# Optimization experiments

Hardware: AMD Instinct MI355X
Metric: run time of the kernel (lower is better)

Reference implementation:

```python
import jax, jax.numpy as jnp
import numpy as np

D_PAIR = 128
D_HIDDEN = 128
EPS = 1e-5


def layer_norm(x, w, b):
    mu = jnp.mean(x, axis=-1, keepdims=True)
    var = jnp.var(x, axis=-1, keepdims=True)
    return (x - mu) * jax.lax.rsqrt(var + EPS) * w + b


def setup_inputs() -> dict:
    key = jax.random.key(0)
    ks = jax.random.split(key, 8)
    B, N, D, H = 1, 512, D_PAIR, D_HIDDEN
    pair = jax.random.normal(ks[0], (B, N, N, D), dtype=jnp.float32)
    # torch Linear weight layout: [out_features, in_features]
    p_in_w = jax.random.normal(ks[1], (2 * H, D), dtype=jnp.float32) / np.sqrt(D)
    g_in_w = jax.random.normal(ks[2], (2 * H, D), dtype=jnp.float32) / np.sqrt(D)
    p_out_w = jax.random.normal(ks[3], (D, H), dtype=jnp.float32) / np.sqrt(H)
    g_out_w = jax.random.normal(ks[4], (D, D), dtype=jnp.float32) / np.sqrt(D)
    ln_in_w = jnp.ones((D,), jnp.float32)
    ln_in_b = jnp.zeros((D,), jnp.float32)
    ln_out_w = jnp.ones((H,), jnp.float32)
    ln_out_b = jnp.zeros((H,), jnp.float32)
    return {
        "pair": pair,
        "ln_in_w": ln_in_w, "ln_in_b": ln_in_b,
        "p_in_w": p_in_w, "g_in_w": g_in_w,
        "ln_out_w": ln_out_w, "ln_out_b": ln_out_b,
        "p_out_w": p_out_w, "g_out_w": g_out_w,
    }


def reference(pair, ln_in_w, ln_in_b, p_in_w, g_in_w, ln_out_w, ln_out_b, p_out_w, g_out_w):
    H = D_HIDDEN
    L = pair.shape[1]
    pair_norm = layer_norm(pair, ln_in_w, ln_in_b)           # [B,N,N,D]
    p = jnp.einsum('bijd,hd->bijh', pair_norm, p_in_w)       # [B,N,N,2H]
    g = jax.nn.sigmoid(jnp.einsum('bijd,hd->bijh', pair_norm, g_in_w))
    left = g[..., :H] * p[..., :H]
    right = g[..., H:] * p[..., H:]
    # outgoing direction
    out = jnp.einsum('bikd,bjkd->bijd', left, right / jnp.float32(L))
    out = layer_norm(out, ln_out_w, ln_out_b)
    out = jnp.einsum('bijh,dh->bijd', out, p_out_w)
    gate = jax.nn.sigmoid(jnp.einsum('bijd,ed->bije', pair_norm, g_out_w))
    return gate * out
```

## Files before the change

kernel.cpp:

```cpp
#include <hip/hip_runtime.h>

#define NSEQ 512
#define RTOT (NSEQ*NSEQ)
#define DM 128

typedef unsigned short ushort_t;
using short8 = __attribute__((ext_vector_type(8))) short;
using f32x4  = __attribute__((ext_vector_type(4))) float;

__device__ __forceinline__ unsigned short f2bf(float x){
  union { float f; unsigned int u; } v; v.f = x;
  unsigned int r = v.u + 0x7fffu + ((v.u >> 16) & 1u);
  return (unsigned short)(r >> 16);
}
__device__ __forceinline__ float bf2f(unsigned short u){
  union { unsigned int u; float f; } v; v.u = ((unsigned int)u) << 16;
  return v.f;
}
__device__ __forceinline__ unsigned int pack2(float a, float b){
  return (unsigned int)f2bf(a) | ((unsigned int)f2bf(b) << 16);
}
__device__ __forceinline__ float sigmoidf(float x){ return 1.0f/(1.0f + __expf(-x)); }

__global__ __launch_bounds__(256) void k_prep(const float* __restrict__ a,
                                              const float* __restrict__ b,
                                              ushort_t* __restrict__ da,
                                              ushort_t* __restrict__ db,
                                              int na4, int nb4){
  int idx = blockIdx.x*256 + threadIdx.x;
  const float* src; ushort_t* dst; int i;
  if (idx < na4){ src = a; dst = da; i = idx; }
  else { i = idx - na4; if (i >= nb4) return; src = b; dst = db; }
  float4 v = *(const float4*)(src + (size_t)i*4);
  uint2 pk; pk.x = pack2(v.x, v.y); pk.y = pack2(v.z, v.w);
  *(uint2*)(dst + (size_t)i*4) = pk;
}

__global__ __launch_bounds__(256) void k_prep2(const float* __restrict__ p_out_w,
                                               const float* __restrict__ g_out_w,
                                               const float* __restrict__ ln_out_w,
                                               const float* __restrict__ ln_out_b,
                                               ushort_t* __restrict__ wp,
                                               ushort_t* __restrict__ wg,
                                               float2* __restrict__ c12){
  int t = threadIdx.x;
  if (t < 128){
    float s1 = 0.f, s2 = 0.f;
    for (int d = 0; d < DM; d++){
      float v = p_out_w[(size_t)t*DM + d];
      unsigned short h = f2bf(v * ln_out_w[d]);
      wp[(size_t)t*DM + d] = h;
      s1 += bf2f(h);
      s2 += ln_out_b[d] * v;
    }
    c12[t] = make_float2(s1, s2);
  } else {
    int r = t - 128;
    for (int d = 0; d < DM; d += 4){
      float4 v = *(const float4*)&g_out_w[(size_t)r*DM + d];
      uint2 pk; pk.x = pack2(v.x, v.y); pk.y = pack2(v.z, v.w);
      *(uint2*)&wg[(size_t)r*DM + d] = pk;
    }
  }
}

__global__ __launch_bounds__(256) void k0_ln_in(const float* __restrict__ pair,
                                                const float* __restrict__ w,
                                                const float* __restrict__ b,
                                                ushort_t* __restrict__ lnx){
  int wv = threadIdx.x >> 6, lane = threadIdx.x & 63;
  size_t row = (size_t)blockIdx.x * 4 + wv;
  const float2* src = (const float2*)(pair + row * DM);
  float2 v = src[lane];
  float s = v.x + v.y, s2 = v.x*v.x + v.y*v.y;
  #pragma unroll
  for (int off = 32; off; off >>= 1){ s += __shfl_xor(s, off); s2 += __shfl_xor(s2, off); }
  float mu = s * (1.f/DM);
  float rstd = rsqrtf(s2*(1.f/DM) - mu*mu + 1e-5f);
  float o0 = (v.x - mu)*rstd*w[2*lane]   + b[2*lane];
  float o1 = (v.y - mu)*rstd*w[2*lane+1] + b[2*lane+1];
  ((unsigned int*)(lnx + row * DM))[lane] = pack2(o0, o1);
}

__global__ __launch_bounds__(256) void k1_inproj(const ushort_t* __restrict__ lnx,
                                                 const ushort_t* __restrict__ pw_bf,
                                                 const ushort_t* __restrict__ gw_bf,
                                                 ushort_t* __restrict__ left,
                                                 ushort_t* __restrict__ right){
  int tid = threadIdx.x;
  int wc = tid >> 6, lane = tid & 63, m = lane & 15, quad = lane >> 4;
  int job = blockIdx.x;
  int wrow0 = ((job >= 2) ? 128 : 0) + (job & 1) * 64;
  ushort_t* outp = (job >= 2) ? right : left;
  int d = (job & 1) * 64 + wc*16 + m;
  size_t row0 = (size_t)blockIdx.y * 256;

  const ushort_t* prow = pw_bf + (size_t)(wrow0 + wc*16 + m)*DM + quad*8;
  const ushort_t* grow = gw_bf + (size_t)(wrow0 + wc*16 + m)*DM + quad*8;
  short8 bp[4], bg[4];
  #pragma unroll
  for (int k = 0; k < 4; k++){
    bp[k] = *(const short8*)(prow + k*32);
    bg[k] = *(const short8*)(grow + k*32);
  }

  #pragma unroll
  for (int ch = 0; ch < 4; ch++){
    size_t r0 = row0 + ch*64;
    f32x4 accp[4], accg[4];
    #pragma unroll
    for (int i = 0; i < 4; i++){ accp[i] = (f32x4){0.f,0.f,0.f,0.f}; accg[i] = (f32x4){0.f,0.f,0.f,0.f}; }
    #pragma unroll
    for (int k = 0; k < 4; k++){
      #pragma unroll
      for (int rt = 0; rt < 4; rt++){
        short8 a = *(const short8*)&lnx[(r0 + rt*16 + m)*DM + k*32 + quad*8];
        accp[rt] = __builtin_amdgcn_mfma_f32_16x16x32_bf16(a, bp[k], accp[rt], 0, 0, 0);
        accg[rt] = __builtin_amdgcn_mfma_f32_16x16x32_bf16(a, bg[k], accg[rt], 0, 0, 0);
      }
    }
    #pragma unroll
    for (int rt = 0; rt < 4; rt++){
      uint2 pk;
      pk.x = pack2(sigmoidf(accg[rt][0])*accp[rt][0], sigmoidf(accg[rt][1])*accp[rt][1]);
      pk.y = pack2(sigmoidf(accg[rt][2])*accp[rt][2], sigmoidf(accg[rt][3])*accp[rt][3]);
      *(uint2*)&outp[(size_t)d * RTOT + r0 + rt*16 + quad*4] = pk;
    }
  }
}

__global__ __launch_bounds__(256) void k2_tri(const ushort_t* __restrict__ left,
                                              const ushort_t* __restrict__ right,
                                              ushort_t* __restrict__ tri){
  __shared__ __align__(16) ushort_t As[128][72];
  __shared__ __align__(16) ushort_t Bs[128][72];
  int tid = threadIdx.x;
  int b = blockIdx.x;
  int d = b & 127, ti = b >> 7;
  const ushort_t* Ap = left  + (size_t)d * RTOT;
  const ushort_t* Bp = right + (size_t)d * RTOT;
  ushort_t* Cp = tri + (size_t)d * RTOT;
  int i0 = ti * 128;
  int w = tid >> 6, lane = tid & 63, m = lane & 15, quad = lane >> 4;
  int wr = w & 1, wc = w >> 1;

  for (int tj = 0; tj < 4; tj++){
    int j0 = tj * 128;
    f32x4 acc[16];
    #pragma unroll
    for (int x = 0; x < 16; x++) acc[x] = (f32x4){0.f,0.f,0.f,0.f};

    for (int kt = 0; kt < NSEQ; kt += 64){
      __syncthreads();
      #pragma unroll
      for (int it = 0; it < 4; it++){
        int e = (tid + it*256) * 8; int r = e >> 6, c = e & 63;
        *(uint4*)&As[r][c] = *(const uint4*)&Ap[(size_t)(i0 + r)*NSEQ + kt + c];
        *(uint4*)&Bs[r][c] = *(const uint4*)&Bp[(size_t)(j0 + r)*NSEQ + kt + c];
      }
      __syncthreads();
      #pragma unroll
      for (int kk = 0; kk < 64; kk += 32){
        short8 a[4], bb[4];
        #pragma unroll
        for (int t = 0; t < 4; t++) a[t]  = *(const short8*)&As[wr*64 + t*16 + m][kk + quad*8];
        #pragma unroll
        for (int c = 0; c < 4; c++) bb[c] = *(const short8*)&Bs[wc*64 + c*16 + m][kk + quad*8];
        #pragma unroll
        for (int t = 0; t < 4; t++){
          #pragma unroll
          for (int c = 0; c < 4; c++){
            acc[t*4+c] = __builtin_amdgcn_mfma_f32_16x16x32_bf16(a[t], bb[c], acc[t*4+c], 0, 0, 0);
          }
        }
      }
    }
    const float s = 1.f / (float)NSEQ;
    #pragma unroll
    for (int t = 0; t < 4; t++){
      #pragma unroll
      for (int c = 0; c < 4; c++){
        int col = j0 + wc*64 + c*16 + m;
        #pragma unroll
        for (int rr = 0; rr < 4; rr++){
          int row = i0 + wr*64 + t*16 + quad*4 + rr;
          Cp[(size_t)row * NSEQ + col] = f2bf(acc[t*4+c][rr] * s);
        }
      }
    }
  }
}

__global__ __launch_bounds__(256) void k3_out(const ushort_t* __restrict__ tri,
                                              const ushort_t* __restrict__ lnx,
                                              const ushort_t* __restrict__ wp,
                                              const ushort_t* __restrict__ wg,
                                              const float2* __restrict__ c12,
                                              float* __restrict__ out){
  __shared__ __align__(16) ushort_t A1[64][136];
  __shared__ __align__(16) ushort_t Bt[64][136];
  __shared__ float ss[64][4], sq[64][4];
  __shared__ float2 srow[64];
  __shared__ float2 c12s[128];
  int tid = threadIdx.x;
  size_t r0 = (size_t)blockIdx.x * 64;
  if (tid < 128) c12s[tid] = c12[tid];

  int j = tid & 63, wv = tid >> 6;
  {
    float fs = 0.f, fq = 0.f;
    #pragma unroll
    for (int g = 0; g < 4; g++){
      int oct = wv*4 + g;
      const ushort_t* src = tri + (size_t)(oct*8)*RTOT + r0 + j;
      short8 v;
      #pragma unroll
      for (int dd = 0; dd < 8; dd++){
        unsigned short u = src[(size_t)dd * RTOT];
        v[dd] = (short)u;
        float f = bf2f(u); fs += f; fq += f*f;
      }
      *(short8*)&A1[j][oct*8] = v;
    }
    ss[j][wv] = fs; sq[j][wv] = fq;
  }
  __syncthreads();
  if (tid < 64){
    float s = ss[tid][0]+ss[tid][1]+ss[tid][2]+ss[tid][3];
    float q = sq[tid][0]+sq[tid][1]+sq[tid][2]+sq[tid][3];
    float mu = s * (1.f/DM);
    float rstd = rsqrtf(q*(1.f/DM) - mu*mu + 1e-5f);
    srow[tid] = make_float2(mu, rstd);
  }
  __syncthreads();

  int lane = tid & 63, m = lane & 15, quad = lane >> 4;
  short8 a1[4], a2[4];
  #pragma unroll
  for (int k = 0; k < 4; k++){
    a1[k] = *(const short8*)&A1[wv*16 + m][k*32 + quad*8];
    a2[k] = *(const short8*)&lnx[(r0 + wv*16 + m)*DM + k*32 + quad*8];
  }
  float2 st[4];
  #pragma unroll
  for (int rr = 0; rr < 4; rr++) st[rr] = srow[wv*16 + quad*4 + rr];

  #pragma unroll
  for (int ch = 0; ch < 2; ch++){
    f32x4 accp[4], accg[4];
    #pragma unroll
    for (int i = 0; i < 4; i++){ accp[i] = (f32x4){0.f,0.f,0.f,0.f}; accg[i] = (f32x4){0.f,0.f,0.f,0.f}; }

    #pragma unroll
    for (int it = 0; it < 4; it++){
      int e = (tid + it*256) * 8; int r = e >> 7, c = e & 127;
      *(uint4*)&Bt[r][c] = *(const uint4*)&wp[(size_t)(ch*64 + r)*DM + c];
    }
    __syncthreads();
    #pragma unroll
    for (int k = 0; k < 4; k++){
      #pragma unroll
      for (int c = 0; c < 4; c++){
        short8 bf = *(const short8*)&Bt[c*16 + m][k*32 + quad*8];
        accp[c] = __builtin_amdgcn_mfma_f32_16x16x32_bf16(a1[k], bf, accp[c], 0, 0, 0);
      }
    }
    __syncthreads();
    #pragma unroll
    for (int it = 0; it < 4; it++){
      int e = (tid + it*256) * 8; int r = e >> 7, c = e & 127;
      *(uint4*)&Bt[r][c] = *(const uint4*)&wg[(size_t)(ch*64 + r)*DM + c];
    }
    __syncthreads();
    #pragma unroll
    for (int k = 0; k < 4; k++){
      #pragma unroll
      for (int c = 0; c < 4; c++){
        short8 bf = *(const short8*)&Bt[c*16 + m][k*32 + quad*8];
        accg[c] = __builtin_amdgcn_mfma_f32_16x16x32_bf16(a2[k], bf, accg[c], 0, 0, 0);
      }
    }
    #pragma unroll
    for (int c = 0; c < 4; c++){
      int h = ch*64 + c*16 + m;
      float2 cc = c12s[h];
      #pragma unroll
      for (int rr = 0; rr < 4; rr++){
        float val = st[rr].y * (accp[c][rr] - st[rr].x * cc.x) + cc.y;
        out[(r0 + wv*16 + quad*4 + rr)*DM + h] = sigmoidf(accg[c][rr]) * val;
      }
    }
    __syncthreads();
  }
}

extern "C" void kernel_launch(void* const* d_in, const int* in_sizes, int n_in,
                              void* d_out, int out_size, void* d_ws, size_t ws_size,
                              hipStream_t stream){
  const float* pair     = (const float*)d_in[0];
  const float* ln_in_w  = (const float*)d_in[1];
  const float* ln_in_b  = (const float*)d_in[2];
  const float* p_in_w   = (const float*)d_in[3];
  const float* g_in_w   = (const float*)d_in[4];
  const float* ln_out_w = (const float*)d_in[5];
  const float* ln_out_b = (const float*)d_in[6];
  const float* p_out_w  = (const float*)d_in[7];
  const float* g_out_w  = (const float*)d_in[8];
  float* out = (float*)d_out;

  const size_t plane = (size_t)RTOT * DM;
  ushort_t* lnx   = (ushort_t*)d_ws;
  ushort_t* left  = lnx   + plane;
  ushort_t* right = left  + plane;
  ushort_t* tri   = right + plane;

  ushort_t* pw_bf = tri;
  ushort_t* gw_bf = tri + 32768;
  ushort_t* wp    = left;
  ushort_t* wg    = left + 16384;
  float2*   c12   = (float2*)(left + 32768);

  k_prep   <<<dim3(64),          dim3(256), 0, stream>>>(p_in_w, g_in_w, pw_bf, gw_bf, 8192, 8192);
  k0_ln_in <<<dim3(RTOT/4),      dim3(256), 0, stream>>>(pair, ln_in_w, ln_in_b, lnx);
  k1_inproj<<<dim3(4, RTOT/256), dim3(256), 0, stream>>>(lnx, pw_bf, gw_bf, left, right);
  k2_tri   <<<dim3(512),         dim3(256), 0, stream>>>(left, right, tri);
  k_prep2  <<<dim3(1),           dim3(256), 0, stream>>>(p_out_w, g_out_w, ln_out_w, ln_out_b, wp, wg, c12);
  k3_out   <<<dim3(RTOT/64),     dim3(256), 0, stream>>>(tri, lnx, wp, wg, c12, out);
}
```

Baseline: 525.2 us.

## Tile input projection through LDS and parallelize output weight prep

The input projection kernel now gives each block 128 rows. It stages the lnx tile once in LDS and keeps it in registers, then loops over four weight groups staged in LDS, computing all 256 projection columns per block. Before, the same lnx rows were re-read from global memory for each of four column jobs. Separately, the single-block output-weight prep kernel is spread over 40 blocks, with a wave reduction replacing the serial per-thread loops. The trade-off is higher register and LDS use per block (about 70KB of LDS) and extra barriers.

```diff
diff --git a/kernel.cpp b/kernel.cpp
--- a/kernel.cpp
+++ b/kernel.cpp
@@ -43,24 +43,30 @@
                                                ushort_t* __restrict__ wp,
                                                ushort_t* __restrict__ wg,
                                                float2* __restrict__ c12){
-  int t = threadIdx.x;
-  if (t < 128){
+  int b = blockIdx.x, tid = threadIdx.x;
+  if (b < 8){
+    int i = b*2048 + tid*8;
+    float4 v0 = *(const float4*)&g_out_w[i];
+    float4 v1 = *(const float4*)&g_out_w[i+4];
+    uint2 p0; p0.x = pack2(v0.x, v0.y); p0.y = pack2(v0.z, v0.w);
+    uint2 p1; p1.x = pack2(v1.x, v1.y); p1.y = pack2(v1.z, v1.w);
+    *(uint2*)&wg[i]   = p0;
+    *(uint2*)&wg[i+4] = p1;
+  } else {
+    int r = (b-8)*4 + (tid>>6), lane = tid & 63;
     float s1 = 0.f, s2 = 0.f;
-    for (int d = 0; d < DM; d++){
-      float v = p_out_w[(size_t)t*DM + d];
+    #pragma unroll
+    for (int t = 0; t < 2; t++){
+      int d = lane + t*64;
+      float v = p_out_w[(size_t)r*DM + d];
       unsigned short h = f2bf(v * ln_out_w[d]);
-      wp[(size_t)t*DM + d] = h;
+      wp[(size_t)r*DM + d] = h;
       s1 += bf2f(h);
       s2 += ln_out_b[d] * v;
     }
-    c12[t] = make_float2(s1, s2);
-  } else {
-    int r = t - 128;
-    for (int d = 0; d < DM; d += 4){
-      float4 v = *(const float4*)&g_out_w[(size_t)r*DM + d];
-      uint2 pk; pk.x = pack2(v.x, v.y); pk.y = pack2(v.z, v.w);
-      *(uint2*)&wg[(size_t)r*DM + d] = pk;
-    }
+    #pragma unroll
+    for (int off = 32; off; off >>= 1){ s1 += __shfl_xor(s1, off); s2 += __shfl_xor(s2, off); }
+    if (lane == 0) c12[r] = make_float2(s1, s2);
   }
 }
 
@@ -87,44 +93,77 @@
                                                  const ushort_t* __restrict__ gw_bf,
                                                  ushort_t* __restrict__ left,
                                                  ushort_t* __restrict__ right){
+  __shared__ __align__(16) ushort_t A[128][136];
+  __shared__ __align__(16) ushort_t B[128][136];
   int tid = threadIdx.x;
-  int wc = tid >> 6, lane = tid & 63, m = lane & 15, quad = lane >> 4;
-  int job = blockIdx.x;
-  int wrow0 = ((job >= 2) ? 128 : 0) + (job & 1) * 64;
-  ushort_t* outp = (job >= 2) ? right : left;
-  int d = (job & 1) * 64 + wc*16 + m;
-  size_t row0 = (size_t)blockIdx.y * 256;
-
-  const ushort_t* prow = pw_bf + (size_t)(wrow0 + wc*16 + m)*DM + quad*8;
-  const ushort_t* grow = gw_bf + (size_t)(wrow0 + wc*16 + m)*DM + quad*8;
-  short8 bp[4], bg[4];
-  #pragma unroll
-  for (int k = 0; k < 4; k++){
-    bp[k] = *(const short8*)(prow + k*32);
-    bg[k] = *(const short8*)(grow + k*32);
-  }
-
-  #pragma unroll
-  for (int ch = 0; ch < 4; ch++){
-    size_t r0 = row0 + ch*64;
-    f32x4 accp[4], accg[4];
-    #pragma unroll
-    for (int i = 0; i < 4; i++){ accp[i] = (f32x4){0.f,0.f,0.f,0.f}; accg[i] = (f32x4){0.f,0.f,0.f,0.f}; }
+  int w = tid >> 6, lane = tid & 63, m = lane & 15, quad = lane >> 4;
+  int wr = w & 1;
+  int wc = w >> 1;
+  size_t row0 = (size_t)blockIdx.x * 128;
+
+  #pragma unroll
+  for (int it = 0; it < 8; it++){
+    int e = (tid + it*256) * 8; int r = e >> 7, c = e & 127;
+    *(uint4*)&A[r][c] = *(const uint4*)&lnx[(row0 + r)*DM + c];
+  }
+  __syncthreads();
+  short8 a[4][4];
+  #pragma unroll
+  for (int rt = 0; rt < 4; rt++)
+    #pragma unroll
+    for (int k = 0; k < 4; k++)
+      a[rt][k] = *(const short8*)&A[wr*64 + rt*16 + m][k*32 + quad*8];
+
+  for (int g = 0; g < 4; g++){
+    __syncthreads();
+    #pragma unroll
+    for (int it = 0; it < 8; it++){
+      int e = (tid + it*256) * 8; int r = e >> 7, c = e & 127;
+      const ushort_t* srcw = (r < 64) ? &pw_bf[(size_t)(g*64 + r)*DM + c]
+                                      : &gw_bf[(size_t)(g*64 + r - 64)*DM + c];
+      *(uint4*)&B[r][c] = *(const uint4*)srcw;
+    }
+    __syncthreads();
+
+    f32x4 accp[4][2], accg[4][2];
+    #pragma unroll
+    for (int rt = 0; rt < 4; rt++)
+      #pragma unroll
+      for (int ct = 0; ct < 2; ct++){
+        accp[rt][ct] = (f32x4){0.f,0.f,0.f,0.f};
+        accg[rt][ct] = (f32x4){0.f,0.f,0.f,0.f};
+      }
     #pragma unroll
     for (int k = 0; k < 4; k++){
+      short8 bp[2], bg[2];
+      #pragma unroll
+      for (int ct = 0; ct < 2; ct++){
+        bp[ct] = *(const short8*)&B[     wc*32 + ct*16 + m][k*32 + quad*8];
+        bg[ct] = *(const short8*)&B[64 + wc*32 + ct*16 + m][k*32 + quad*8];
+      }
       #pragma unroll
       for (int rt = 0; rt < 4; rt++){
-        short8 a = *(const short8*)&lnx[(r0 + rt*16 + m)*DM + k*32 + quad*8];
-        accp[rt] = __builtin_amdgcn_mfma_f32_16x16x32_bf16(a, bp[k], accp[rt], 0, 0, 0);
-        accg[rt] = __builtin_amdgcn_mfma_f32_16x16x32_bf16(a, bg[k], accg[rt], 0, 0, 0);
-      }
-    }
-    #pragma unroll
-    for (int rt = 0; rt < 4; rt++){
-      uint2 pk;
-      pk.x = pack2(sigmoidf(accg[rt][0])*accp[rt][0], sigmoidf(accg[rt][1])*accp[rt][1]);
-      pk.y = pack2(sigmoidf(accg[rt][2])*accp[rt][2], sigmoidf(accg[rt][3])*accp[rt][3]);
-      *(uint2*)&outp[(size_t)d * RTOT + r0 + rt*16 + quad*4] = pk;
+        #pragma unroll
+        for (int ct = 0; ct < 2; ct++){
+          accp[rt][ct] = __builtin_amdgcn_mfma_f32_16x16x32_bf16(a[rt][k], bp[ct], accp[rt][ct], 0, 0, 0);
+          accg[rt][ct] = __builtin_amdgcn_mfma_f32_16x16x32_bf16(a[rt][k], bg[ct], accg[rt][ct], 0, 0, 0);
+        }
+      }
+    }
+    ushort_t* outp = (g < 2) ? left : right;
+    int dbase = (g & 1) * 64 + wc*32;
+    #pragma unroll
+    for (int ct = 0; ct < 2; ct++){
+      int d = dbase + ct*16 + m;
+      #pragma unroll
+      for (int rt = 0; rt < 4; rt++){
+        uint2 pk;
+        pk.x = pack2(sigmoidf(accg[rt][ct][0])*accp[rt][ct][0],
+                     sigmoidf(accg[rt][ct][1])*accp[rt][ct][1]);
+        pk.y = pack2(sigmoidf(accg[rt][ct][2])*accp[rt][ct][2],
+                     sigmoidf(accg[rt][ct][3])*accp[rt][ct][3]);
+        *(uint2*)&outp[(size_t)d * RTOT + row0 + wr*64 + rt*16 + quad*4] = pk;
+      }
     }
   }
 }
@@ -320,10 +359,10 @@
   ushort_t* wg    = left + 16384;
   float2*   c12   = (float2*)(left + 32768);
 
-  k_prep   <<<dim3(64),          dim3(256), 0, stream>>>(p_in_w, g_in_w, pw_bf, gw_bf, 8192, 8192);
-  k0_ln_in <<<dim3(RTOT/4),      dim3(256), 0, stream>>>(pair, ln_in_w, ln_in_b, lnx);
-  k1_inproj<<<dim3(4, RTOT/256), dim3(256), 0, stream>>>(lnx, pw_bf, gw_bf, left, right);
-  k2_tri   <<<dim3(512),         dim3(256), 0, stream>>>(left, right, tri);
-  k_prep2  <<<dim3(1),           dim3(256), 0, stream>>>(p_out_w, g_out_w, ln_out_w, ln_out_b, wp, wg, c12);
-  k3_out   <<<dim3(RTOT/64),     dim3(256), 0, stream>>>(tri, lnx, wp, wg, c12, out);
-}
+  k_prep   <<<dim3(64),        dim3(256), 0, stream>>>(p_in_w, g_in_w, pw_bf, gw_bf, 8192, 8192);
+  k0_ln_in <<<dim3(RTOT/4),    dim3(256), 0, stream>>>(pair, ln_in_w, ln_in_b, lnx);
+  k1_inproj<<<dim3(RTOT/128),  dim3(256), 0, stream>>>(lnx, pw_bf, gw_bf, left, right);
+  k2_tri   <<<dim3(512),       dim3(256), 0, stream>>>(left, right, tri);
+  k_prep2  <<<dim3(40),        dim3(256), 0, stream>>>(p_out_w, g_out_w, ln_out_w, ln_out_b, wp, wg, c12);
+  k3_out   <<<dim3(RTOT/64),   dim3(256), 0, stream>>>(tri, lnx, wp, wg, c12, out);
+}
```

Result: faster. 448.8 us (-14.5%).
